# Kernel tuning notes

Measured on AMD Instinct MI355X. Metric: run time of the kernel, lower is better.

The kernel has to match this reference:

```python
import jax, jax.numpy as jnp
import numpy as np

MARGIN = 1.0


def setup_inputs() -> dict:
    key = jax.random.key(0)
    k1, k2, k3 = jax.random.split(key, 3)
    N, F = 4096, 512
    a = jax.random.normal(k1, (N, F), dtype=jnp.float32)
    b = jax.random.normal(k2, (N, F), dtype=jnp.float32)
    labels = jax.random.randint(k3, (N,), 0, 16, dtype=jnp.int32)
    return {"a": a, "b": b, "labels": labels}


def reference(a, b, labels):
    # D[i, j] = ||b_i - a_j||  (torch: Xa=a[None], Xb=b[:,None], sum over feat)
    # GEMM form of the pairwise sqdist; clamp tiny fp negatives before sqrt.
    Dsq = (jnp.sum(b * b, axis=1)[:, None]
           + jnp.sum(a * a, axis=1)[None, :]
           - 2.0 * (b @ a.T))
    D = jnp.sqrt(jnp.maximum(Dsq, 0.0))            # [N, N]
    Dexpm = jnp.exp(MARGIN - D)                    # [N, N]

    same = labels[:, None] == labels[None, :]      # [N, N]
    eye = jnp.eye(labels.shape[0], dtype=bool)
    pos_mask = same & ~eye                         # ordered positive pairs (i, j)
    neg_mask = ~same                               # negative pairs (labels differ)

    # neg_i sum for row i: sum_k Dexpm[i, k] over k with labels[k] != labels[i]
    row_negsum = jnp.sum(jnp.where(neg_mask, Dexpm, 0.0), axis=1)  # [N]

    # J_ij = log(neg_ik_sum + neg_jl_sum) + D[i, j]; hinged and squared
    J = jnp.log(row_negsum[:, None] + row_negsum[None, :]) + D
    hinge_sq = jnp.square(jnp.maximum(J, 0.0))

    num_pos = jnp.sum(pos_mask)
    return jnp.sum(jnp.where(pos_mask, hinge_sq, 0.0)) / (2.0 * num_pos)
```

## Files before the change

kernel.cpp:

```cpp
#include <hip/hip_runtime.h>
#include <math.h>

#define NROW 4096
#define FDIM 512
#define MARGIN 1.0f

typedef __attribute__((ext_vector_type(8))) short short8;
typedef __attribute__((ext_vector_type(4))) float floatx4;

__device__ inline unsigned short f2bf(float x) {
    unsigned u = __float_as_uint(x);
    return (unsigned short)((u + 0x7FFFu + ((u >> 16) & 1u)) >> 16);
}
__device__ inline float h2f(unsigned short u) {
    _Float16 h; __builtin_memcpy(&h, &u, 2); return (float)h;
}
__device__ inline unsigned short f2h(float f) {
    _Float16 h = (_Float16)f; unsigned short u; __builtin_memcpy(&u, &h, 2); return u;
}

__global__ __launch_bounds__(64) void prep_kernel(
    const float* __restrict__ a, const float* __restrict__ b,
    unsigned short* __restrict__ abf, unsigned short* __restrict__ bbf,
    float* __restrict__ na, float* __restrict__ nb,
    float* __restrict__ rns, float* __restrict__ loss) {
    int row  = blockIdx.x;
    int lane = threadIdx.x;
    const float4* a4 = (const float4*)(a + (size_t)row * FDIM);
    const float4* b4 = (const float4*)(b + (size_t)row * FDIM);
    ushort4* au = (ushort4*)(abf + (size_t)row * FDIM);
    ushort4* bu = (ushort4*)(bbf + (size_t)row * FDIM);
    float sa = 0.f, sb = 0.f;
    #pragma unroll
    for (int f = lane; f < FDIM / 4; f += 64) {
        float4 va = a4[f];
        float4 vb = b4[f];
        sa += va.x * va.x + va.y * va.y + va.z * va.z + va.w * va.w;
        sb += vb.x * vb.x + vb.y * vb.y + vb.z * vb.z + vb.w * vb.w;
        ushort4 ua = { f2bf(va.x), f2bf(va.y), f2bf(va.z), f2bf(va.w) };
        ushort4 ub = { f2bf(vb.x), f2bf(vb.y), f2bf(vb.z), f2bf(vb.w) };
        au[f] = ua;
        bu[f] = ub;
    }
    #pragma unroll
    for (int o = 32; o > 0; o >>= 1) {
        sa += __shfl_down(sa, o);
        sb += __shfl_down(sb, o);
    }
    if (lane == 0) {
        na[row] = sa;
        nb[row] = sb;
        rns[row] = 0.f;
        if (row == 0) loss[0] = 0.f;
    }
}

template <int MODE>
__global__ __launch_bounds__(256) void pass_mfma(
    const unsigned short* __restrict__ abf, const unsigned short* __restrict__ bbf,
    const int* __restrict__ labels,
    const float* __restrict__ na, const float* __restrict__ nb,
    float* __restrict__ rns, unsigned short* __restrict__ Dws,
    float* __restrict__ loss_sum)
{
    __shared__ __align__(16) unsigned short arena[17408];
    __shared__ int   li_s[128], lj_s[128];
    __shared__ float nb_s[128], na_s[128], rbi_s[128], rbj_s[128];

    const int t    = threadIdx.x;
    const int lane = t & 63;
    const int w    = t >> 6;
    const int wi   = w >> 1, wj = w & 1;
    const int bid  = blockIdx.x;
    const int sup  = bid >> 6, loc = bid & 63;
    const int by   = ((sup >> 2) << 3) | (loc >> 3);
    const int bx   = ((sup & 3) << 3) | (loc & 7);
    const int ti   = by * 128;
    const int tj   = bx * 128;
    const int lr   = lane & 15;
    const int lq   = lane >> 4;

    floatx4 acc[4][4];
    #pragma unroll
    for (int i = 0; i < 4; ++i)
        #pragma unroll
        for (int j = 0; j < 4; ++j)
            acc[i][j] = (floatx4){0.f, 0.f, 0.f, 0.f};

    if (t < 128) {
        li_s[t] = labels[ti + t];
        nb_s[t] = nb[ti + t];
        if (MODE == 2) rbi_s[t] = rns[ti + t];
    } else {
        int u = t - 128;
        lj_s[u] = labels[tj + u];
        na_s[u] = na[tj + u];
        if (MODE == 2) rbj_s[u] = rns[tj + u];
    }

    auto stage = [&](int kk, int buf) {
        unsigned short* As = arena + buf * 8192;
        unsigned short* Bs = arena + 4096 + buf * 8192;
        #pragma unroll
        for (int l = 0; l < 2; ++l) {
            int c   = t + l * 256;
            int row = c >> 2;
            int q   = c & 3;
            size_t ga = (size_t)(tj + row) * FDIM + kk + q * 8;
            size_t gb = (size_t)(ti + row) * FDIM + kk + q * 8;
            __builtin_amdgcn_global_load_lds(
                (const __attribute__((address_space(1))) unsigned int*)(abf + ga),
                (__attribute__((address_space(3))) unsigned int*)(As + c * 8), 16, 0, 0);
            __builtin_amdgcn_global_load_lds(
                (const __attribute__((address_space(1))) unsigned int*)(bbf + gb),
                (__attribute__((address_space(3))) unsigned int*)(Bs + c * 8), 16, 0, 0);
        }
    };

    stage(0, 0);
    __syncthreads();

    #pragma unroll
    for (int it = 0; it < FDIM / 32; ++it) {
        if (it < FDIM / 32 - 1) stage((it + 1) * 32, (it + 1) & 1);

        const unsigned short* As = arena + (it & 1) * 8192;
        const unsigned short* Bs = arena + 4096 + (it & 1) * 8192;
        short8 af[4], bf[4];
        #pragma unroll
        for (int ri = 0; ri < 4; ++ri)
            af[ri] = *(const short8*)&Bs[(wi * 64 + ri * 16 + lr) * 32 + lq * 8];
        #pragma unroll
        for (int rj = 0; rj < 4; ++rj)
            bf[rj] = *(const short8*)&As[(wj * 64 + rj * 16 + lr) * 32 + lq * 8];
        #pragma unroll
        for (int ri = 0; ri < 4; ++ri)
            #pragma unroll
            for (int rj = 0; rj < 4; ++rj)
                acc[ri][rj] = __builtin_amdgcn_mfma_f32_16x16x32_bf16(
                    af[ri], bf[rj], acc[ri][rj], 0, 0, 0);

        __syncthreads();
    }

    if (MODE == 0 || MODE == 1) {
        unsigned short* D_s = arena;
        #pragma unroll
        for (int ri = 0; ri < 4; ++ri) {
            float rs[4] = {0.f, 0.f, 0.f, 0.f};
            #pragma unroll
            for (int rj = 0; rj < 4; ++rj) {
                int   jl  = wj * 64 + rj * 16 + lr;
                float naj = na_s[jl];
                int   ljv = lj_s[jl];
                #pragma unroll
                for (int r = 0; r < 4; ++r) {
                    int   il  = wi * 64 + ri * 16 + lq * 4 + r;
                    float dsq = nb_s[il] + naj - 2.f * acc[ri][rj][r];
                    float D   = sqrtf(fmaxf(dsq, 0.f));
                    if (li_s[il] != ljv) rs[r] += __expf(MARGIN - D);
                    if (MODE == 0) D_s[il * 136 + jl] = f2h(D);
                }
            }
            #pragma unroll
            for (int r = 0; r < 4; ++r) {
                #pragma unroll
                for (int o = 8; o > 0; o >>= 1) rs[r] += __shfl_down(rs[r], o, 16);
            }
            if (lr == 0) {
                #pragma unroll
                for (int r = 0; r < 4; ++r)
                    atomicAdd(&rns[ti + wi * 64 + ri * 16 + lq * 4 + r], rs[r]);
            }
        }
        if (MODE == 0) {
            __syncthreads();
            #pragma unroll
            for (int l = 0; l < 8; ++l) {
                int c  = t + l * 256;
                int r  = c >> 4;
                int cw = c & 15;
                *(short8*)&Dws[(size_t)(ti + r) * NROW + tj + cw * 8] =
                    *(const short8*)&D_s[r * 136 + cw * 8];
            }
        }
    } else {
        float local = 0.f;
        #pragma unroll
        for (int ri = 0; ri < 4; ++ri)
            #pragma unroll
            for (int rj = 0; rj < 4; ++rj) {
                int jl  = wj * 64 + rj * 16 + lr;
                int ljv = lj_s[jl];
                float naj = na_s[jl], rbj = rbj_s[jl];
                #pragma unroll
                for (int r = 0; r < 4; ++r) {
                    int il = wi * 64 + ri * 16 + lq * 4 + r;
                    int i  = ti + il, j = tj + jl;
                    if (li_s[il] == ljv && i != j) {
                        float dsq = nb_s[il] + naj - 2.f * acc[ri][rj][r];
                        float D   = sqrtf(fmaxf(dsq, 0.f));
                        float J   = __logf(rbi_s[il] + rbj) + D;
                        float h   = fmaxf(J, 0.f);
                        local += h * h;
                    }
                }
            }
        #pragma unroll
        for (int o = 32; o > 0; o >>= 1) local += __shfl_down(local, o);
        __shared__ float part[4];
        if (lane == 0) part[w] = local;
        __syncthreads();
        if (t == 0) atomicAdd(loss_sum, part[0] + part[1] + part[2] + part[3]);
    }
}

__global__ __launch_bounds__(256) void pass2_sweep(
    const unsigned short* __restrict__ Dws, const int* __restrict__ labels,
    const float* __restrict__ rns, float* __restrict__ loss_sum)
{
    const int t = threadIdx.x;
    float local = 0.f;
    #pragma unroll
    for (int l = 0; l < 4; ++l) {
        int c  = blockIdx.x * 256 + t + l * 524288;
        int i  = c >> 9;
        int j0 = (c & 511) * 8;
        int   li  = labels[i];
        float rbi = rns[i];
        short8 d8 = *(const short8*)&Dws[(size_t)i * NROW + j0];
        int4   la = *(const int4*)&labels[j0];
        int4   lb = *(const int4*)&labels[j0 + 4];
        float4 ra = *(const float4*)&rns[j0];
        float4 rb = *(const float4*)&rns[j0 + 4];
        int   labs[8] = {la.x, la.y, la.z, la.w, lb.x, lb.y, lb.z, lb.w};
        float rnsj[8] = {ra.x, ra.y, ra.z, ra.w, rb.x, rb.y, rb.z, rb.w};
        #pragma unroll
        for (int e = 0; e < 8; ++e) {
            int j = j0 + e;
            if (labs[e] == li && j != i) {
                float J = __logf(rbi + rnsj[e]) + h2f((unsigned short)d8[e]);
                float h = fmaxf(J, 0.f);
                local += h * h;
            }
        }
    }
    #pragma unroll
    for (int o = 32; o > 0; o >>= 1) local += __shfl_down(local, o);
    __shared__ float part[4];
    if ((t & 63) == 0) part[t >> 6] = local;
    __syncthreads();
    if (t == 0) atomicAdd(loss_sum, part[0] + part[1] + part[2] + part[3]);
}

__global__ __launch_bounds__(256) void finalize_kernel(const int* __restrict__ labels,
                                                       const float* __restrict__ loss_sum,
                                                       float* __restrict__ out) {
    __shared__ int hist[16];
    int t = threadIdx.x;
    if (t < 16) hist[t] = 0;
    __syncthreads();
    for (int i = t; i < NROW; i += 256) atomicAdd(&hist[labels[i] & 15], 1);
    __syncthreads();
    if (t == 0) {
        long long np = 0;
        for (int c = 0; c < 16; ++c) np += (long long)hist[c] * (long long)(hist[c] - 1);
        out[0] = loss_sum[0] / (2.0f * (float)np);
    }
}

extern "C" void kernel_launch(void* const* d_in, const int* in_sizes, int n_in,
                              void* d_out, int out_size, void* d_ws, size_t ws_size,
                              hipStream_t stream) {
    const float* a      = (const float*)d_in[0];
    const float* b      = (const float*)d_in[1];
    const int*   labels = (const int*)d_in[2];
    float* out = (float*)d_out;

    unsigned short* abf = (unsigned short*)d_ws;
    unsigned short* bbf = abf + (size_t)NROW * FDIM;
    float* fws  = (float*)(bbf + (size_t)NROW * FDIM);
    float* na   = fws;
    float* nb   = fws + NROW;
    float* rns  = fws + 2 * NROW;
    float* loss = fws + 3 * NROW;
    unsigned short* Dws = (unsigned short*)(fws + 3 * NROW + 4);

    size_t need = ((char*)Dws - (char*)d_ws) + (size_t)NROW * NROW * 2;

    prep_kernel<<<NROW, 64, 0, stream>>>(a, b, abf, bbf, na, nb, rns, loss);

    dim3 grid((NROW / 128) * (NROW / 128));
    if (ws_size >= need) {
        pass_mfma<0><<<grid, 256, 0, stream>>>(abf, bbf, labels, na, nb, rns, Dws, loss);
        pass2_sweep<<<2048, 256, 0, stream>>>(Dws, labels, rns, loss);
    } else {
        pass_mfma<1><<<grid, 256, 0, stream>>>(abf, bbf, labels, na, nb, rns, Dws, loss);
        pass_mfma<2><<<grid, 256, 0, stream>>>(abf, bbf, labels, na, nb, rns, Dws, loss);
    }

    finalize_kernel<<<1, 256, 0, stream>>>(labels, loss, out);
}
```

Before: 146.1 us.

## Load MFMA operands directly from global memory instead of LDS staging

Replaces the double-buffered global-to-LDS staging loop with direct per-lane 16-byte global loads of the bf16 operand fragments, feeding the MFMAs straight from registers. This removes the per-iteration barrier and LDS traffic, with a single sync left before the epilogue. The trade-off is that operand reuse across waves now relies on L1/L2 caches rather than shared memory, which raises global load traffic and may expose memory latency without explicit prefetch.

```diff
diff --git a/kernel.cpp b/kernel.cpp
--- a/kernel.cpp
+++ b/kernel.cpp
@@ -98,50 +98,31 @@
         if (MODE == 2) rbj_s[u] = rns[tj + u];
     }
 
-    auto stage = [&](int kk, int buf) {
-        unsigned short* As = arena + buf * 8192;
-        unsigned short* Bs = arena + 4096 + buf * 8192;
-        #pragma unroll
-        for (int l = 0; l < 2; ++l) {
-            int c   = t + l * 256;
-            int row = c >> 2;
-            int q   = c & 3;
-            size_t ga = (size_t)(tj + row) * FDIM + kk + q * 8;
-            size_t gb = (size_t)(ti + row) * FDIM + kk + q * 8;
-            __builtin_amdgcn_global_load_lds(
-                (const __attribute__((address_space(1))) unsigned int*)(abf + ga),
-                (__attribute__((address_space(3))) unsigned int*)(As + c * 8), 16, 0, 0);
-            __builtin_amdgcn_global_load_lds(
-                (const __attribute__((address_space(1))) unsigned int*)(bbf + gb),
-                (__attribute__((address_space(3))) unsigned int*)(Bs + c * 8), 16, 0, 0);
-        }
-    };
-
-    stage(0, 0);
-    __syncthreads();
-
-    #pragma unroll
-    for (int it = 0; it < FDIM / 32; ++it) {
-        if (it < FDIM / 32 - 1) stage((it + 1) * 32, (it + 1) & 1);
-
-        const unsigned short* As = arena + (it & 1) * 8192;
-        const unsigned short* Bs = arena + 4096 + (it & 1) * 8192;
+    const unsigned short* bbase[4];
+    const unsigned short* abase[4];
+    #pragma unroll
+    for (int ri = 0; ri < 4; ++ri)
+        bbase[ri] = bbf + (size_t)(ti + wi * 64 + ri * 16 + lr) * FDIM + lq * 8;
+    #pragma unroll
+    for (int rj = 0; rj < 4; ++rj)
+        abase[rj] = abf + (size_t)(tj + wj * 64 + rj * 16 + lr) * FDIM + lq * 8;
+
+    #pragma unroll 2
+    for (int kk = 0; kk < FDIM; kk += 32) {
         short8 af[4], bf[4];
         #pragma unroll
-        for (int ri = 0; ri < 4; ++ri)
-            af[ri] = *(const short8*)&Bs[(wi * 64 + ri * 16 + lr) * 32 + lq * 8];
-        #pragma unroll
-        for (int rj = 0; rj < 4; ++rj)
-            bf[rj] = *(const short8*)&As[(wj * 64 + rj * 16 + lr) * 32 + lq * 8];
+        for (int ri = 0; ri < 4; ++ri) af[ri] = *(const short8*)(bbase[ri] + kk);
+        #pragma unroll
+        for (int rj = 0; rj < 4; ++rj) bf[rj] = *(const short8*)(abase[rj] + kk);
         #pragma unroll
         for (int ri = 0; ri < 4; ++ri)
             #pragma unroll
             for (int rj = 0; rj < 4; ++rj)
                 acc[ri][rj] = __builtin_amdgcn_mfma_f32_16x16x32_bf16(
                     af[ri], bf[rj], acc[ri][rj], 0, 0, 0);
-
-        __syncthreads();
-    }
+    }
+
+    __syncthreads();
 
     if (MODE == 0 || MODE == 1) {
         unsigned short* D_s = arena;
```

After: 190.7 us. 30.6% more time.

## Store D in per-block MFMA fragment order and sweep it tile-wise

Applied to the files above, without the earlier changes.

The pass-1 epilogue now writes each thread's fp16 distances straight to global memory in accumulator-fragment order, one contiguous 16 KB chunk per tile. This drops the LDS staging transpose and its extra barrier, and the arena shrinks to 16384 shorts. Pass 2 now launches one block per tile, reads the same fragment layout, and caches the tile's labels and row sums in shared memory so it no longer reloads them per row from global memory. The cost is that per-element index mapping is recomputed in pass 2, and both kernels must agree exactly on the layout.

```diff
diff --git a/kernel.cpp b/kernel.cpp
--- a/kernel.cpp
+++ b/kernel.cpp
@@ -17,6 +17,11 @@
 }
 __device__ inline unsigned short f2h(float f) {
     _Float16 h = (_Float16)f; unsigned short u; __builtin_memcpy(&u, &h, 2); return u;
+}
+__device__ inline void glds16(const unsigned short* g, unsigned short* l) {
+    __builtin_amdgcn_global_load_lds(
+        (const __attribute__((address_space(1))) unsigned int*)g,
+        (__attribute__((address_space(3))) unsigned int*)l, 16, 0, 0);
 }
 
 __global__ __launch_bounds__(64) void prep_kernel(
@@ -63,7 +68,7 @@
     float* __restrict__ rns, unsigned short* __restrict__ Dws,
     float* __restrict__ loss_sum)
 {
-    __shared__ __align__(16) unsigned short arena[17408];
+    __shared__ __align__(16) unsigned short arena[16384];
     __shared__ int   li_s[128], lj_s[128];
     __shared__ float nb_s[128], na_s[128], rbi_s[128], rbj_s[128];
 
@@ -106,14 +111,8 @@
             int c   = t + l * 256;
             int row = c >> 2;
             int q   = c & 3;
-            size_t ga = (size_t)(tj + row) * FDIM + kk + q * 8;
-            size_t gb = (size_t)(ti + row) * FDIM + kk + q * 8;
-            __builtin_amdgcn_global_load_lds(
-                (const __attribute__((address_space(1))) unsigned int*)(abf + ga),
-                (__attribute__((address_space(3))) unsigned int*)(As + c * 8), 16, 0, 0);
-            __builtin_amdgcn_global_load_lds(
-                (const __attribute__((address_space(1))) unsigned int*)(bbf + gb),
-                (__attribute__((address_space(3))) unsigned int*)(Bs + c * 8), 16, 0, 0);
+            glds16(abf + (size_t)(tj + row) * FDIM + kk + q * 8, As + c * 8);
+            glds16(bbf + (size_t)(ti + row) * FDIM + kk + q * 8, Bs + c * 8);
         }
     };
 
@@ -125,7 +124,7 @@
         if (it < FDIM / 32 - 1) stage((it + 1) * 32, (it + 1) & 1);
 
         const unsigned short* As = arena + (it & 1) * 8192;
-        const unsigned short* Bs = arena + 4096 + (it & 1) * 8192;
+        const unsigned short* Bs = As + 4096;
         short8 af[4], bf[4];
         #pragma unroll
         for (int ri = 0; ri < 4; ++ri)
@@ -139,15 +138,15 @@
             for (int rj = 0; rj < 4; ++rj)
                 acc[ri][rj] = __builtin_amdgcn_mfma_f32_16x16x32_bf16(
                     af[ri], bf[rj], acc[ri][rj], 0, 0, 0);
-
         __syncthreads();
     }
 
     if (MODE == 0 || MODE == 1) {
-        unsigned short* D_s = arena;
+        unsigned short* dblk = Dws + (size_t)bid * 16384;
         #pragma unroll
         for (int ri = 0; ri < 4; ++ri) {
             float rs[4] = {0.f, 0.f, 0.f, 0.f};
+            unsigned short dloc[16];
             #pragma unroll
             for (int rj = 0; rj < 4; ++rj) {
                 int   jl  = wj * 64 + rj * 16 + lr;
@@ -159,7 +158,7 @@
                     float dsq = nb_s[il] + naj - 2.f * acc[ri][rj][r];
                     float D   = sqrtf(fmaxf(dsq, 0.f));
                     if (li_s[il] != ljv) rs[r] += __expf(MARGIN - D);
-                    if (MODE == 0) D_s[il * 136 + jl] = f2h(D);
+                    if (MODE == 0) dloc[rj * 4 + r] = f2h(D);
                 }
             }
             #pragma unroll
@@ -172,16 +171,9 @@
                 for (int r = 0; r < 4; ++r)
                     atomicAdd(&rns[ti + wi * 64 + ri * 16 + lq * 4 + r], rs[r]);
             }
-        }
-        if (MODE == 0) {
-            __syncthreads();
-            #pragma unroll
-            for (int l = 0; l < 8; ++l) {
-                int c  = t + l * 256;
-                int r  = c >> 4;
-                int cw = c & 15;
-                *(short8*)&Dws[(size_t)(ti + r) * NROW + tj + cw * 8] =
-                    *(const short8*)&D_s[r * 136 + cw * 8];
+            if (MODE == 0) {
+                *(short8*)&dblk[(ri * 2 + 0) * 2048 + t * 8] = *(short8*)&dloc[0];
+                *(short8*)&dblk[(ri * 2 + 1) * 2048 + t * 8] = *(short8*)&dloc[8];
             }
         }
     } else {
@@ -219,36 +211,60 @@
     const unsigned short* __restrict__ Dws, const int* __restrict__ labels,
     const float* __restrict__ rns, float* __restrict__ loss_sum)
 {
-    const int t = threadIdx.x;
+    __shared__ int   lab_i[128], lab_j[128];
+    __shared__ float rb_i[128], rb_j[128];
+
+    const int t    = threadIdx.x;
+    const int lane = t & 63;
+    const int w    = t >> 6;
+    const int wi   = w >> 1, wj = w & 1;
+    const int bid  = blockIdx.x;
+    const int sup  = bid >> 6, loc = bid & 63;
+    const int by   = ((sup >> 2) << 3) | (loc >> 3);
+    const int bx   = ((sup & 3) << 3) | (loc & 7);
+    const int ti   = by * 128;
+    const int tj   = bx * 128;
+    const int lr   = lane & 15;
+    const int lq   = lane >> 4;
+
+    if (t < 128) {
+        lab_i[t] = labels[ti + t];
+        rb_i[t]  = rns[ti + t];
+    } else {
+        int u = t - 128;
+        lab_j[u] = labels[tj + u];
+        rb_j[u]  = rns[tj + u];
+    }
+    __syncthreads();
+
+    const unsigned short* dblk = Dws + (size_t)bid * 16384;
     float local = 0.f;
     #pragma unroll
-    for (int l = 0; l < 4; ++l) {
-        int c  = blockIdx.x * 256 + t + l * 524288;
-        int i  = c >> 9;
-        int j0 = (c & 511) * 8;
-        int   li  = labels[i];
-        float rbi = rns[i];
-        short8 d8 = *(const short8*)&Dws[(size_t)i * NROW + j0];
-        int4   la = *(const int4*)&labels[j0];
-        int4   lb = *(const int4*)&labels[j0 + 4];
-        float4 ra = *(const float4*)&rns[j0];
-        float4 rb = *(const float4*)&rns[j0 + 4];
-        int   labs[8] = {la.x, la.y, la.z, la.w, lb.x, lb.y, lb.z, lb.w};
-        float rnsj[8] = {ra.x, ra.y, ra.z, ra.w, rb.x, rb.y, rb.z, rb.w};
-        #pragma unroll
-        for (int e = 0; e < 8; ++e) {
-            int j = j0 + e;
-            if (labs[e] == li && j != i) {
-                float J = __logf(rbi + rnsj[e]) + h2f((unsigned short)d8[e]);
-                float h = fmaxf(J, 0.f);
-                local += h * h;
+    for (int ri = 0; ri < 4; ++ri) {
+        short8 d0 = *(const short8*)&dblk[(ri * 2 + 0) * 2048 + t * 8];
+        short8 d1 = *(const short8*)&dblk[(ri * 2 + 1) * 2048 + t * 8];
+        #pragma unroll
+        for (int rj = 0; rj < 4; ++rj) {
+            int jl  = wj * 64 + rj * 16 + lr;
+            int ljv = lab_j[jl];
+            #pragma unroll
+            for (int r = 0; r < 4; ++r) {
+                int il = wi * 64 + ri * 16 + lq * 4 + r;
+                if (lab_i[il] == ljv && (ti + il) != (tj + jl)) {
+                    unsigned short du = (rj < 2)
+                        ? (unsigned short)d0[rj * 4 + r]
+                        : (unsigned short)d1[(rj - 2) * 4 + r];
+                    float J = __logf(rb_i[il] + rb_j[jl]) + h2f(du);
+                    float h = fmaxf(J, 0.f);
+                    local += h * h;
+                }
             }
         }
     }
     #pragma unroll
     for (int o = 32; o > 0; o >>= 1) local += __shfl_down(local, o);
     __shared__ float part[4];
-    if ((t & 63) == 0) part[t >> 6] = local;
+    if (lane == 0) part[w] = local;
     __syncthreads();
     if (t == 0) atomicAdd(loss_sum, part[0] + part[1] + part[2] + part[3]);
 }
@@ -293,7 +309,7 @@
     dim3 grid((NROW / 128) * (NROW / 128));
     if (ws_size >= need) {
         pass_mfma<0><<<grid, 256, 0, stream>>>(abf, bbf, labels, na, nb, rns, Dws, loss);
-        pass2_sweep<<<2048, 256, 0, stream>>>(Dws, labels, rns, loss);
+        pass2_sweep<<<grid, 256, 0, stream>>>(Dws, labels, rns, loss);
     } else {
         pass_mfma<1><<<grid, 256, 0, stream>>>(abf, bbf, labels, na, nb, rns, Dws, loss);
         pass_mfma<2><<<grid, 256, 0, stream>>>(abf, bbf, labels, na, nb, rns, Dws, loss);
```

Result: faster. 135.5 us (median of 2 runs) (-7.3%).
